# Kernel tuning notes

Hardware: AMD Instinct MI355X
Metric: run time of the kernel (lower is better)

The kernel has to match this reference:

```python
import jax, jax.numpy as jnp
import numpy as np

B, C, H, W = 4, 64, 128, 128
KH, KW = 5, 5
PAD = 2
HEADS, DIM_HEAD = 8, 8


def setup_inputs() -> dict:
    key = jax.random.key(0)
    k1, k2, k3, k4 = jax.random.split(key, 4)
    return {
        "features1": jax.random.normal(k1, (B, C, H, W), dtype=jnp.float32),
        "features2": jax.random.normal(k2, (B, C, H, W), dtype=jnp.float32),
        "rel_h": jax.random.normal(k3, (C // 2, 1, 1, KH, 1), dtype=jnp.float32),
        "rel_w": jax.random.normal(k4, (C // 2, 1, 1, 1, KW), dtype=jnp.float32),
    }


def reference(features1, features2, rel_h, rel_w):
    b, c, h, w = features1.shape
    K = KH * KW
    # pad key/value source spatially
    padded = jnp.pad(features2, ((0, 0), (0, 0), (PAD, PAD), (PAD, PAD)))
    # materialize sliding windows: [B, C, H, W, KH*KW], kw index minor (matches torch unfold(2).unfold(3))
    windows = jnp.stack(
        [padded[:, :, i:i + h, j:j + w] for i in range(KH) for j in range(KW)],
        axis=-1,
    )
    # relative position bias: first C/2 channels get rel_h, last C/2 get rel_w
    relh = jnp.broadcast_to(rel_h.reshape(c // 2, KH, 1), (c // 2, KH, KW))
    relw = jnp.broadcast_to(rel_w.reshape(c // 2, 1, KW), (c // 2, KH, KW))
    rel = jnp.concatenate([relh, relw], axis=0).reshape(c, K)  # [C, K]
    k = windows + rel[None, :, None, None, :]
    v = windows
    q = features1.reshape(b, HEADS, DIM_HEAD, h, w, 1)
    k = k.reshape(b, HEADS, DIM_HEAD, h, w, K)
    v = v.reshape(b, HEADS, DIM_HEAD, h, w, K)
    # per-channel windowed softmax attention (no reduction over channel in scores)
    attn = jax.nn.softmax(q * k, axis=-1)
    # einsum 'abcdef,abcdef->acbde' from torch: output is [B, dim_head, heads, H, W]
    out = jnp.einsum('bhcxyk,bhcxyk->bchxy', attn, v)
    return out.reshape(b, c, h, w)
```

## Files before the change

kernel.cpp:

```cpp
#include <hip/hip_runtime.h>

#define B_ 4
#define C_ 64
#define H_ 128
#define W_ 128
#define LOG2E 1.44269504088896340736f

typedef float v2f __attribute__((ext_vector_type(2)));

__device__ __forceinline__ v2f exp2v(v2f x) {
    return (v2f){ __builtin_amdgcn_exp2f(x.x), __builtin_amdgcn_exp2f(x.y) };
}

template<int HALF>
__device__ __forceinline__ void sa_body(int x0, int y0,
    const float* __restrict__ f1p, const float* __restrict__ f2p,
    const float* __restrict__ relp, float* __restrict__ outp)
{
    float rel5[5];
    #pragma unroll
    for (int k = 0; k < 5; ++k) rel5[k] = relp[k];

    const float mL = (x0 > 0) ? 1.0f : 0.0f;
    const float mR = (x0 < W_ - 4) ? 1.0f : 0.0f;
    const int eM = (x0 >= 4) ? x0 - 4 : 0;
    const int eC = x0;
    const int eP = (x0 <= W_ - 8) ? x0 + 4 : W_ - 4;

    float w[5][8];

    auto load_row = [&](int slot, int ky) {
        const int kycl = ky < 0 ? 0 : (ky > H_ - 1 ? H_ - 1 : ky);
        const float rv = ((unsigned)ky < (unsigned)H_) ? 1.0f : 0.0f;
        const float* rp = f2p + kycl * W_;
        const float4 qm = *(const float4*)(rp + eM);
        const float4 q0 = *(const float4*)(rp + eC);
        const float4 qp = *(const float4*)(rp + eP);
        const float mLr = mL * rv, mRr = mR * rv;
        w[slot][0] = qm.z * mLr; w[slot][1] = qm.w * mLr;
        w[slot][2] = q0.x * rv;  w[slot][3] = q0.y * rv;
        w[slot][4] = q0.z * rv;  w[slot][5] = q0.w * rv;
        w[slot][6] = qp.x * mRr; w[slot][7] = qp.y * mRr;
    };

    #pragma unroll
    for (int t = 0; t < 4; ++t) load_row(t, y0 + t - 2);

    #pragma unroll
    for (int r = 0; r < 4; ++r) {
        load_row((r + 4) % 5, y0 + r + 2);

        const float4 q4 = *(const float4*)(f1p + (y0 + r) * W_ + x0);
        const float qs[4] = {q4.x, q4.y, q4.z, q4.w};
        float res[4];

        #pragma unroll
        for (int xo = 0; xo < 4; ++xo) {
            const float q2 = qs[xo] * LOG2E;
            const v2f q2v = {q2, q2};

            float pr[5];
            #pragma unroll
            for (int k = 0; k < 5; ++k) pr[k] = q2 * rel5[k];
            const v2f prA = {pr[0], pr[1]};
            const v2f prB = {pr[2], pr[3]};
            const float prC = pr[4];

            v2f s0 = {0.f, 0.f}, s1 = {0.f, 0.f};
            v2f d0 = {0.f, 0.f}, d1 = {0.f, 0.f};
            float lv[5];

            #pragma unroll
            for (int i = 0; i < 5; ++i) {
                const float* W8 = w[(r + i) % 5];
                const v2f va = {W8[xo + 0], W8[xo + 1]};
                const v2f vb = {W8[xo + 2], W8[xo + 3]};
                const v2f pa = (HALF == 0) ? (v2f){pr[i], pr[i]} : prA;
                const v2f pb = (HALF == 0) ? (v2f){pr[i], pr[i]} : prB;
                const v2f p0 = exp2v(__builtin_elementwise_fma(va, q2v, pa));
                s0 += p0; d0 = __builtin_elementwise_fma(p0, va, d0);
                const v2f p1 = exp2v(__builtin_elementwise_fma(vb, q2v, pb));
                s1 += p1; d1 = __builtin_elementwise_fma(p1, vb, d1);
                lv[i] = W8[xo + 4];
            }
            {
                const v2f v = {lv[0], lv[1]};
                const v2f pp = (HALF == 0) ? (v2f){pr[0], pr[1]} : (v2f){prC, prC};
                const v2f p = exp2v(__builtin_elementwise_fma(v, q2v, pp));
                s0 += p; d0 = __builtin_elementwise_fma(p, v, d0);
            }
            {
                const v2f v = {lv[2], lv[3]};
                const v2f pp = (HALF == 0) ? (v2f){pr[2], pr[3]} : (v2f){prC, prC};
                const v2f p = exp2v(__builtin_elementwise_fma(v, q2v, pp));
                s1 += p; d1 = __builtin_elementwise_fma(p, v, d1);
            }
            float ss, ds;
            {
                const float pp = (HALF == 0) ? pr[4] : prC;
                const float p = __builtin_amdgcn_exp2f(__builtin_fmaf(q2, lv[4], pp));
                ss = p; ds = p * lv[4];
            }
            const v2f st = s0 + s1, dt = d0 + d1;
            const float sum = st.x + st.y + ss;
            const float dot = dt.x + dt.y + ds;
            res[xo] = dot * __builtin_amdgcn_rcpf(sum);
        }

        *(float4*)(outp + (y0 + r) * W_ + x0) = (float4){res[0], res[1], res[2], res[3]};
    }
}

__global__ __launch_bounds__(256) void sa_kernel(
    const float* __restrict__ f1, const float* __restrict__ f2,
    const float* __restrict__ relh, const float* __restrict__ relw,
    float* __restrict__ out)
{
    const int tid   = threadIdx.x;
    const int xq    = tid & 31;
    const int ys    = tid >> 5;
    const int blk   = blockIdx.x;
    const int chunk = blk & 3;
    const int bc    = blk >> 2;
    const int c     = bc & (C_ - 1);
    const int b     = bc >> 6;
    const int x0    = xq << 2;
    const int y0    = chunk * 32 + ys * 4;

    const size_t img = (size_t)(b * C_ + c) * (H_ * W_);
    const float* f1p = f1 + img;
    const float* f2p = f2 + img;

    const int c_out = (c & 7) * 8 + (c >> 3);
    float* outp = out + (size_t)(b * C_ + c_out) * (H_ * W_);

    if (c < C_ / 2) sa_body<0>(x0, y0, f1p, f2p, relh + c * 5, outp);
    else            sa_body<1>(x0, y0, f1p, f2p, relw + (c - C_ / 2) * 5, outp);
}

extern "C" void kernel_launch(void* const* d_in, const int* in_sizes, int n_in,
                              void* d_out, int out_size, void* d_ws, size_t ws_size,
                              hipStream_t stream) {
    const float* f1   = (const float*)d_in[0];
    const float* f2   = (const float*)d_in[1];
    const float* relh = (const float*)d_in[2];
    const float* relw = (const float*)d_in[3];
    float* out = (float*)d_out;

    const int grid = B_ * C_ * 4;
    sa_kernel<<<grid, 256, 0, stream>>>(f1, f2, relh, relw, out);
}
```

Measured before the change: 21.65 us.

## Halve rows per thread, double grid, and preload all window rows upfront

Each thread now computes 2 output rows instead of 4, so the grid doubles to 2048 blocks. All 6 needed feature2 rows and both feature1 rows are loaded before any compute, and launch bounds now request 6 waves per SIMD. This aims for more parallelism, occupancy and memory-level parallelism. The cost is more redundant halo loads per output, with each row reused over 2 outputs rather than 4.

New measurement: 59.31 us. 2.74x slower.

```diff
diff --git a/kernel.cpp b/kernel.cpp
--- a/kernel.cpp
+++ b/kernel.cpp
@@ -24,34 +24,30 @@
     const float mL = (x0 > 0) ? 1.0f : 0.0f;
     const float mR = (x0 < W_ - 4) ? 1.0f : 0.0f;
     const int eM = (x0 >= 4) ? x0 - 4 : 0;
-    const int eC = x0;
     const int eP = (x0 <= W_ - 8) ? x0 + 4 : W_ - 4;
 
-    float w[5][8];
-
-    auto load_row = [&](int slot, int ky) {
+    float w[6][8];
+    #pragma unroll
+    for (int t = 0; t < 6; ++t) {
+        const int ky = y0 + t - 2;
         const int kycl = ky < 0 ? 0 : (ky > H_ - 1 ? H_ - 1 : ky);
         const float rv = ((unsigned)ky < (unsigned)H_) ? 1.0f : 0.0f;
         const float* rp = f2p + kycl * W_;
         const float4 qm = *(const float4*)(rp + eM);
-        const float4 q0 = *(const float4*)(rp + eC);
+        const float4 q0 = *(const float4*)(rp + x0);
         const float4 qp = *(const float4*)(rp + eP);
         const float mLr = mL * rv, mRr = mR * rv;
-        w[slot][0] = qm.z * mLr; w[slot][1] = qm.w * mLr;
-        w[slot][2] = q0.x * rv;  w[slot][3] = q0.y * rv;
-        w[slot][4] = q0.z * rv;  w[slot][5] = q0.w * rv;
-        w[slot][6] = qp.x * mRr; w[slot][7] = qp.y * mRr;
-    };
+        w[t][0] = qm.z * mLr; w[t][1] = qm.w * mLr;
+        w[t][2] = q0.x * rv;  w[t][3] = q0.y * rv;
+        w[t][4] = q0.z * rv;  w[t][5] = q0.w * rv;
+        w[t][6] = qp.x * mRr; w[t][7] = qp.y * mRr;
+    }
+    const float4 qrow[2] = { *(const float4*)(f1p + y0 * W_ + x0),
+                             *(const float4*)(f1p + (y0 + 1) * W_ + x0) };
 
     #pragma unroll
-    for (int t = 0; t < 4; ++t) load_row(t, y0 + t - 2);
-
-    #pragma unroll
-    for (int r = 0; r < 4; ++r) {
-        load_row((r + 4) % 5, y0 + r + 2);
-
-        const float4 q4 = *(const float4*)(f1p + (y0 + r) * W_ + x0);
-        const float qs[4] = {q4.x, q4.y, q4.z, q4.w};
+    for (int r = 0; r < 2; ++r) {
+        const float qs[4] = {qrow[r].x, qrow[r].y, qrow[r].z, qrow[r].w};
         float res[4];
 
         #pragma unroll
@@ -72,7 +68,7 @@
 
             #pragma unroll
             for (int i = 0; i < 5; ++i) {
-                const float* W8 = w[(r + i) % 5];
+                const float* W8 = w[r + i];
                 const v2f va = {W8[xo + 0], W8[xo + 1]};
                 const v2f vb = {W8[xo + 2], W8[xo + 3]};
                 const v2f pa = (HALF == 0) ? (v2f){pr[i], pr[i]} : prA;
@@ -84,48 +80,46 @@
                 lv[i] = W8[xo + 4];
             }
             {
-                const v2f v = {lv[0], lv[1]};
+                const v2f v  = {lv[0], lv[1]};
                 const v2f pp = (HALF == 0) ? (v2f){pr[0], pr[1]} : (v2f){prC, prC};
-                const v2f p = exp2v(__builtin_elementwise_fma(v, q2v, pp));
+                const v2f p  = exp2v(__builtin_elementwise_fma(v, q2v, pp));
                 s0 += p; d0 = __builtin_elementwise_fma(p, v, d0);
             }
             {
-                const v2f v = {lv[2], lv[3]};
+                const v2f v  = {lv[2], lv[3]};
                 const v2f pp = (HALF == 0) ? (v2f){pr[2], pr[3]} : (v2f){prC, prC};
-                const v2f p = exp2v(__builtin_elementwise_fma(v, q2v, pp));
+                const v2f p  = exp2v(__builtin_elementwise_fma(v, q2v, pp));
                 s1 += p; d1 = __builtin_elementwise_fma(p, v, d1);
             }
             float ss, ds;
             {
                 const float pp = (HALF == 0) ? pr[4] : prC;
-                const float p = __builtin_amdgcn_exp2f(__builtin_fmaf(q2, lv[4], pp));
+                const float p  = __builtin_amdgcn_exp2f(__builtin_fmaf(q2, lv[4], pp));
                 ss = p; ds = p * lv[4];
             }
             const v2f st = s0 + s1, dt = d0 + d1;
-            const float sum = st.x + st.y + ss;
-            const float dot = dt.x + dt.y + ds;
-            res[xo] = dot * __builtin_amdgcn_rcpf(sum);
+            res[xo] = (dt.x + dt.y + ds) * __builtin_amdgcn_rcpf(st.x + st.y + ss);
         }
 
         *(float4*)(outp + (y0 + r) * W_ + x0) = (float4){res[0], res[1], res[2], res[3]};
     }
 }
 
-__global__ __launch_bounds__(256) void sa_kernel(
+__global__ __launch_bounds__(256, 6) void sa_kernel(
     const float* __restrict__ f1, const float* __restrict__ f2,
     const float* __restrict__ relh, const float* __restrict__ relw,
     float* __restrict__ out)
 {
-    const int tid   = threadIdx.x;
-    const int xq    = tid & 31;
-    const int ys    = tid >> 5;
-    const int blk   = blockIdx.x;
-    const int chunk = blk & 3;
-    const int bc    = blk >> 2;
-    const int c     = bc & (C_ - 1);
-    const int b     = bc >> 6;
-    const int x0    = xq << 2;
-    const int y0    = chunk * 32 + ys * 4;
+    const int tid = threadIdx.x;
+    const int xq  = tid & 31;
+    const int ys  = tid >> 5;
+    const int blk = blockIdx.x;
+    const int by  = blk & 7;
+    const int bc  = blk >> 3;
+    const int c   = bc & (C_ - 1);
+    const int b   = bc >> 6;
+    const int x0  = xq << 2;
+    const int y0  = by * 16 + ys * 2;
 
     const size_t img = (size_t)(b * C_ + c) * (H_ * W_);
     const float* f1p = f1 + img;
@@ -147,6 +141,6 @@
     const float* relw = (const float*)d_in[3];
     float* out = (float*)d_out;
 
-    const int grid = B_ * C_ * 4;
+    const int grid = B_ * C_ * 8;
     sa_kernel<<<grid, 256, 0, stream>>>(f1, f2, relh, relw, out);
 }
```
